# Performance work log

Hardware: AMD Instinct MI355X
Metric: run time of the kernel (lower is better)

## Reference

```python
import jax, jax.numpy as jnp
import numpy as np

B, I, C, H, QP, VP = 2, 1024, 16, 12, 4, 8
W_C = (2.0 / (9.0 * QP)) ** 0.5
W_L = (1.0 / 3.0) ** 0.5


def setup_inputs() -> dict:
    key = jax.random.key(0)
    ks = jax.random.split(key, 14)
    rn = lambda k, shape, s=1.0: (jax.random.normal(k, shape, dtype=jnp.float32) * s)
    return {
        "s": rn(ks[0], (B, I, C)),
        "z": rn(ks[1], (B, I, I, C)),
        "R": rn(ks[2], (B, I, 3, 3)),
        "t": rn(ks[3], (B, I, 3)),
        "Wq": rn(ks[4], (C, C * H), C ** -0.5),
        "Wk": rn(ks[5], (C, C * H), C ** -0.5),
        "Wv": rn(ks[6], (C, C * H), C ** -0.5),
        "Wb": rn(ks[7], (C, H), C ** -0.5),
        "Wqp": rn(ks[8], (C, 3 * QP * H), C ** -0.5),
        "Wkp": rn(ks[9], (C, 3 * QP * H), C ** -0.5),
        "Wvp": rn(ks[10], (C, 3 * VP * H), C ** -0.5),
        "gamma": rn(ks[11], (H,), 0.5),
        "Wout": rn(ks[12], (H * (2 * C + 4 * VP), C), (H * (2 * C + 4 * VP)) ** -0.5),
        "bout": rn(ks[13], (C,), 0.02),
    }


def _apply_rigid(R, t, p):
    # p: (B, i, n, 3); rigid transform per residue: R @ p + t
    return jnp.einsum("bixy,bipy->bipx", R, p) + t[:, :, None, :]


def reference(s, z, R, t, Wq, Wk, Wv, Wb, Wqp, Wkp, Wvp, gamma, Wout, bout):
    b_, i_, c = s.shape
    h, qp, vp = gamma.shape[0], Wqp.shape[1] // (3 * gamma.shape[0]), Wvp.shape[1] // (3 * gamma.shape[0])

    q = (s @ Wq).reshape(b_, i_, h, c)
    k = (s @ Wk).reshape(b_, i_, h, c)
    v = (s @ Wv).reshape(b_, i_, h, c)

    q_pts = _apply_rigid(R, t, (s @ Wqp).reshape(b_, i_, h * qp, 3)).reshape(b_, i_, h, qp, 3)
    k_pts = _apply_rigid(R, t, (s @ Wkp).reshape(b_, i_, h * qp, 3)).reshape(b_, i_, h, qp, 3)
    v_pts = _apply_rigid(R, t, (s @ Wvp).reshape(b_, i_, h * vp, 3)).reshape(b_, i_, h, vp, 3)

    bias = jnp.einsum("bijc,ch->bhij", z, Wb)
    a = jnp.einsum("bihc,bjhc->bhij", q, k) * (c ** -0.5) + bias

    # squared point distances summed over points, expanded to avoid (B,i,j,h,P,3) tensor
    q2 = jnp.sum(q_pts ** 2, axis=(-1, -2))          # (B,i,h)
    k2 = jnp.sum(k_pts ** 2, axis=(-1, -2))          # (B,j,h)
    qk = jnp.einsum("bihpx,bjhpx->bhij", q_pts, k_pts)
    d2 = q2.transpose(0, 2, 1)[..., None] + k2.transpose(0, 2, 1)[:, :, None, :] - 2.0 * qk  # (B,h,i,j)

    head_w = jax.nn.softplus(gamma)                  # (h,)
    a = a + d2 * (head_w[None, :, None, None] * W_C * -0.5)
    a = a * W_L
    a = jax.nn.softmax(a, axis=-2)  # NOTE: original code softmaxes over dim=-2 (the i axis)

    # NOTE: original einsum indexes v by i (not j); replicated faithfully
    o = jnp.einsum("bhij,bihc->bihc", a, v).reshape(b_, i_, h * c)

    o_pts = jnp.einsum("bhij,bjhpx->bihpx", a, v_pts)  # (B,i,h,vp,3)
    o_pts_norm = jnp.sqrt(jnp.maximum(jnp.sum(o_pts ** 2, axis=-1), 1e-12)).reshape(b_, i_, h * vp)
    o_pts_flat = o_pts.reshape(b_, i_, h * vp * 3)

    o_pair = jnp.einsum("bhij,bijc->bihc", a, z).reshape(b_, i_, h * c)

    cat = jnp.concatenate([o, o_pair, o_pts_flat, o_pts_norm], axis=-1)
    return cat @ Wout + bout
```

## Files before the change

### kernel.cpp

```cpp
#include <hip/hip_runtime.h>
#include <hip/hip_bf16.h>
#include <math.h>

#define B_ 2
#define I_ 1024
#define C_ 16
#define H_ 12
#define ICH 8

__device__ __constant__ float kW_C = 0.23570226039551584f;
#define W_Lc 0.5773502691896258f
#define LOG2E 1.4426950408889634f

typedef _Float16 hf;
typedef hf hf2 __attribute__((ext_vector_type(2)));
typedef unsigned int u32;

template <typename T, typename F>
__device__ inline T bc(F f) { return __builtin_bit_cast(T, f); }

__device__ inline float fdot2f(u32 a, u32 b, float c) {
#if __has_builtin(__builtin_amdgcn_fdot2)
  return __builtin_amdgcn_fdot2(bc<hf2>(a), bc<hf2>(b), c, false);
#else
  hf2 x = bc<hf2>(a), y = bc<hf2>(b);
  return c + (float)x[0] * (float)y[0] + (float)x[1] * (float)y[1];
#endif
}

__device__ inline u32 pkrtz(float lo, float hi) {
#if __has_builtin(__builtin_amdgcn_cvt_pkrtz)
  return bc<u32>(__builtin_amdgcn_cvt_pkrtz(lo, hi));
#else
  hf2 t; t[0] = (hf)lo; t[1] = (hf)hi; return bc<u32>(t);
#endif
}

__device__ inline u32 permlo(u32 hiw, u32 low) {
#if __has_builtin(__builtin_amdgcn_perm)
  return __builtin_amdgcn_perm(hiw, low, 0x05040100u);
#else
  return (low & 0xffffu) | (hiw << 16);
#endif
}
__device__ inline u32 permhi(u32 hiw, u32 low) {
#if __has_builtin(__builtin_amdgcn_perm)
  return __builtin_amdgcn_perm(hiw, low, 0x07060302u);
#else
  return (low >> 16) | (hiw & 0xffff0000u);
#endif
}

__device__ inline void ld16lds(const ushort* p, u32* d) {
  const uint4* q = (const uint4*)p;
  uint4 a = q[0], b = q[1], c = q[2], e = q[3];
  d[0]=a.x; d[1]=a.y; d[2]=a.z; d[3]=a.w;
  d[4]=b.x; d[5]=b.y; d[6]=b.z; d[7]=b.w;
  d[8]=c.x; d[9]=c.y; d[10]=c.z; d[11]=c.w;
  d[12]=e.x; d[13]=e.y; d[14]=e.z; d[15]=e.w;
}
__device__ inline void ld8lds(const ushort* p, u32* d) {
  const uint4* q = (const uint4*)p;
  uint4 a = q[0], b = q[1];
  d[0]=a.x; d[1]=a.y; d[2]=a.z; d[3]=a.w;
  d[4]=b.x; d[5]=b.y; d[6]=b.z; d[7]=b.w;
}

#define QF16_OFF 0
#define QF16_SZ (B_*I_*196)
#define KF16_OFF (QF16_OFF + QF16_SZ)
#define KF16_SZ QF16_SZ
#define VPF_OFF (KF16_OFF + KF16_SZ)
#define VPF_SZ (B_*I_*144)
#define VV_OFF (VPF_OFF + VPF_SZ)
#define VV_SZ (B_*I_*192)
#define SM_OFF (VV_OFF + VV_SZ)
#define SM_SZ (B_*12*1024*2)
#define PM_OFF (SM_OFF + SM_SZ)
#define PM_SZ (B_*64*ICH*192*2)
#define LT_OFF (PM_OFF + PM_SZ)
#define LT_SZ (B_*H_*512*1024)
#define ACC2_OFF (LT_OFF + LT_SZ)

__global__ __launch_bounds__(192) void kA(const float* __restrict__ s, const float* __restrict__ R,
                 const float* __restrict__ t, const float* __restrict__ Wq,
                 const float* __restrict__ Wk, const float* __restrict__ Wv,
                 const float* __restrict__ Wqp, const float* __restrict__ Wkp,
                 const float* __restrict__ Wvp, const float* __restrict__ gam,
                 float* __restrict__ ws) {
  int blk = blockIdx.x;
  int b = blk >> 10, i = blk & 1023;
  int tid = threadIdx.x;
  __shared__ float sl[16], rl[9], tl[3], part[96];
  if (tid < 16) sl[tid] = s[(b*I_ + i)*C_ + tid];
  else if (tid < 25) rl[tid-16] = R[(size_t)(b*I_+i)*9 + (tid-16)];
  else if (tid < 28) tl[tid-25] = t[(size_t)(b*I_+i)*3 + (tid-25)];
  __syncthreads();
  hf* QF  = (hf*)(ws + QF16_OFF) + (size_t)(b*I_+i)*392;
  hf* KF  = (hf*)(ws + KF16_OFF) + (size_t)(b*I_+i)*392;
  ushort* VPP = (ushort*)(ws + VPF_OFF);
  float* vv = ws + VV_OFF + (size_t)(b*I_+i)*192;
  {
    int hc = tid; int h = hc >> 4, c = hc & 15;
    float aq = 0.f, ak = 0.f, av = 0.f;
    #pragma unroll
    for (int ci = 0; ci < 16; ci++) {
      float sv = sl[ci];
      aq += sv * Wq[ci*192 + hc];
      ak += sv * Wk[ci*192 + hc];
      av += sv * Wv[ci*192 + hc];
    }
    const float s_qk = 0.25f * W_Lc * LOG2E;
    QF[h*32 + c] = (hf)(aq * s_qk);
    KF[h*32 + c] = (hf)ak;
    vv[hc] = av;
  }
  {
    float raw[3], px[3];
    if (tid < 96) {
      bool isq = tid < 48;
      int n = isq ? tid : tid - 48;
      const float* W = isq ? Wqp : Wkp;
      #pragma unroll
      for (int x = 0; x < 3; x++) {
        float a2 = 0.f;
        #pragma unroll
        for (int ci = 0; ci < 16; ci++) a2 += sl[ci] * W[ci*144 + n*3 + x];
        raw[x] = a2;
      }
      #pragma unroll
      for (int x = 0; x < 3; x++)
        px[x] = rl[x*3]*raw[0] + rl[x*3+1]*raw[1] + rl[x*3+2]*raw[2] + tl[x];
      int h = n >> 2, p = n & 3;
      part[tid] = px[0]*px[0] + px[1]*px[1] + px[2]*px[2];
      if (isq) {
        float g = gam[h];
        float sp = log1pf(expf(g));
        float coef2 = -0.5f * kW_C * sp * W_Lc * LOG2E;
        #pragma unroll
        for (int x = 0; x < 3; x++) QF[h*32 + 16 + p*3 + x] = (hf)(px[x] * (-2.0f * coef2));
      } else {
        #pragma unroll
        for (int x = 0; x < 3; x++) KF[h*32 + 16 + p*3 + x] = (hf)px[x];
      }
    } else {
      int n = tid - 96;
      #pragma unroll
      for (int x = 0; x < 3; x++) {
        float a2 = 0.f;
        #pragma unroll
        for (int ci = 0; ci < 16; ci++) a2 += sl[ci] * Wvp[ci*288 + n*3 + x];
        raw[x] = a2;
      }
      #pragma unroll
      for (int x = 0; x < 3; x++)
        px[x] = rl[x*3]*raw[0] + rl[x*3+1]*raw[1] + rl[x*3+2]*raw[2] + tl[x];
      int h = n >> 3, p = n & 7;
      size_t base = ((size_t)(b*512 + (i >> 1))*12 + h)*48 + (i & 1);
      #pragma unroll
      for (int x = 0; x < 3; x++) VPP[base + (p*3 + x)*2] = bc<ushort>((hf)px[x]);
    }
  }
  __syncthreads();
  if (tid < 24) {
    int h = tid % 12; bool isq = tid < 12;
    float g = gam[h];
    float sp = log1pf(expf(g));
    float coef2 = -0.5f * kW_C * sp * W_Lc * LOG2E;
    float s2 = 0.f;
    int base = isq ? h*4 : 48 + h*4;
    #pragma unroll
    for (int p = 0; p < 4; p++) s2 += part[base + p];
    if (isq) {
      QF[h*32 + 28] = (hf)(coef2 * s2);
      QF[h*32 + 29] = (hf)1.0f;
      QF[h*32 + 30] = (hf)0.0f;
      QF[h*32 + 31] = (hf)0.0f;
    } else {
      KF[h*32 + 28] = (hf)1.0f;
      KF[h*32 + 29] = (hf)(coef2 * s2);
      KF[h*32 + 30] = (hf)0.0f;
      KF[h*32 + 31] = (hf)0.0f;
    }
  }
}

__global__ __launch_bounds__(192,4) void kB(const float* __restrict__ z,
                 const float* __restrict__ Wb, float* __restrict__ ws) {
  int blk = blockIdx.x;
  int ic = blk & (ICH-1); int jt = (blk >> 3) & 63; int b = blk >> 9;
  int tid = threadIdx.x; int h = tid >> 4, jl = tid & 15;
  int j = jt*16 + jl;
  __shared__ ushort qlds[16*392];
  __shared__ ushort zlds[16*392];
  __shared__ u32 llog[96*18];
  u32 kf[16];
  {
    const ushort* KF = (const ushort*)(ws + KF16_OFF) + (size_t)(b*I_+j)*392 + h*32;
    ld16lds(KF, kf);
  }
  u32 wb2[8];
  #pragma unroll
  for (int p = 0; p < 8; p++)
    wb2[p] = pkrtz(Wb[(2*p)*12 + h] * (W_Lc*LOG2E), Wb[(2*p+1)*12 + h] * (W_Lc*LOG2E));
  u32* LTu_w = (u32*)(ws + LT_OFF);
  float m = -1e30f, S = 0.f;
  int ibase = ic*128;
  for (int t = 0; t < 8; ++t) {
    int i0 = ibase + t*16;
    __syncthreads();
    {
      const uint4* qsrc = (const uint4*)((const hf*)(ws + QF16_OFF) + (size_t)(b*I_+i0)*392);
      uint4* qdst = (uint4*)qlds;
      for (int idx = tid; idx < 784; idx += 192) qdst[idx] = qsrc[idx];
    }
    for (int idx = tid; idx < 1024; idx += 192) {
      int r = idx >> 6, jj = (idx >> 2) & 15, c4 = idx & 3;
      float4 v = *(const float4*)(z + ((size_t)(b*I_ + i0 + r)*I_ + jt*16 + jj)*16 + c4*4);
      uint2 pk = make_uint2(pkrtz(v.x, v.y), pkrtz(v.z, v.w));
      *(uint2*)&zlds[r*392 + jj*24 + c4*4] = pk;
    }
    __syncthreads();
    u32 lw[8];
    #pragma unroll 1
    for (int ip = 0; ip < 8; ++ip) {
      u32 q0[16], q1[16], z0[8], z1[8];
      ld16lds(&qlds[(2*ip)*392 + h*32], q0);
      ld16lds(&qlds[(2*ip+1)*392 + h*32], q1);
      ld8lds(&zlds[(2*ip)*392 + jl*24], z0);
      ld8lds(&zlds[(2*ip+1)*392 + jl*24], z1);
      float a0 = 0.f, a1 = 0.f, b0 = 0.f, b1 = 0.f;
      #pragma unroll
      for (int p = 0; p < 16; p += 2) {
        a0 = fdot2f(q0[p], kf[p], a0);
        b0 = fdot2f(q0[p+1], kf[p+1], b0);
        a1 = fdot2f(q1[p], kf[p], a1);
        b1 = fdot2f(q1[p+1], kf[p+1], b1);
      }
      #pragma unroll
      for (int p = 0; p < 8; p += 2) {
        a0 = fdot2f(z0[p], wb2[p], a0);
        b0 = fdot2f(z0[p+1], wb2[p+1], b0);
        a1 = fdot2f(z1[p], wb2[p], a1);
        b1 = fdot2f(z1[p+1], wb2[p+1], b1);
      }
      float l0 = (a0 + b0), l1 = (a1 + b1);
      u32 w = pkrtz(l0, l1);
      lw[ip] = w;
      u32 pw = (u32)__shfl_xor((int)w, 1);
      u32 ex = (jl & 1) ? permhi(w, pw) : permlo(pw, w);
      llog[(h*8 + (jl>>1))*18 + 2*ip + (jl&1)] = ex;
    }
    {
      float l[16];
      #pragma unroll
      for (int p = 0; p < 8; p++) { hf2 lh = bc<hf2>(lw[p]); l[2*p] = (float)lh[0]; l[2*p+1] = (float)lh[1]; }
      float m8[8];
      #pragma unroll
      for (int p = 0; p < 8; p++) m8[p] = fmaxf(l[2*p], l[2*p+1]);
      float mt = fmaxf(fmaxf(fmaxf(m8[0],m8[1]), fmaxf(m8[2],m8[3])),
                       fmaxf(fmaxf(m8[4],m8[5]), fmaxf(m8[6],m8[7])));
      float e[16];
      #pragma unroll
      for (int p = 0; p < 16; p++) e[p] = __builtin_amdgcn_exp2f(l[p] - mt);
      float st = ((e[0]+e[1])+(e[2]+e[3])) + ((e[4]+e[5])+(e[6]+e[7]))
               + ((e[8]+e[9])+(e[10]+e[11])) + ((e[12]+e[13])+(e[14]+e[15]));
      float mn = fmaxf(m, mt);
      S = S * __builtin_amdgcn_exp2f(m - mn) + st * __builtin_amdgcn_exp2f(mt - mn);
      m = mn;
    }
    __syncthreads();
    {
      int row = tid >> 1, iseg = (tid & 1) << 3;
      int hh = row >> 3, jpg2 = row & 7;
      const u32* lr = llog + row*18 + iseg;
      u32 o0=lr[0],o1=lr[1],o2=lr[2],o3=lr[3],o4=lr[4],o5=lr[5],o6=lr[6],o7=lr[7];
      u32* dst = LTu_w + ((size_t)(b*12+hh)*512 + jt*8 + jpg2)*1024 + i0 + iseg;
      *(uint4*)dst = make_uint4(o0,o1,o2,o3);
      *(uint4*)(dst+4) = make_uint4(o4,o5,o6,o7);
    }
  }
  float2* pm = (float2*)(ws + PM_OFF);
  pm[((size_t)(b*64+jt)*ICH + ic)*192 + tid] = make_float2(m, S);
}

__global__ __launch_bounds__(192) void kB2(float* __restrict__ ws) {
  int blk = blockIdx.x; int jt = blk & 63, b = blk >> 6;
  int tid = threadIdx.x; int h = tid >> 4, jl = tid & 15;
  const float2* pm = (const float2*)(ws + PM_OFF) + (size_t)(b*64+jt)*ICH*192 + tid;
  float m = -1e30f, S = 0.f;
  #pragma unroll
  for (int ic = 0; ic < ICH; ic++) {
    float2 p = pm[ic*192];
    float mn = fmaxf(m, p.x);
    S = S * __builtin_amdgcn_exp2f(m - mn) + p.y * __builtin_amdgcn_exp2f(p.x - mn);
    m = mn;
  }
  int j = jt*16 + jl;
  float* sm = ws + SM_OFF + ((size_t)((b*12+h)*1024) + j)*2;
  sm[0] = m;
  sm[1] = 1.0f / S;
}

__global__ __launch_bounds__(192,6) void kC(const float* __restrict__ z,
                 float* __restrict__ ws, int jsh) {
  int blk = blockIdx.x;
  int jch = 1 << jsh;
  int jc = blk & (jch-1); int it = (blk >> jsh) & 63; int b = blk >> (jsh+6);
  int tid = threadIdx.x; int h = tid >> 4, il = tid & 15;
  int i = it*16 + il;
  __shared__ u32 llds[96*18];
  __shared__ u32 zplds[16*132];
  float opts[24], opair[16], rsum = 0.f;
  #pragma unroll
  for (int n = 0; n < 24; n++) opts[n] = 0.f;
  #pragma unroll
  for (int c = 0; c < 16; c++) opair[c] = 0.f;
  const u32* LTu = (const u32*)(ws + LT_OFF);
  const float* SM = ws + SM_OFF + (size_t)((b*12+h)*1024)*2;
  const ushort* VPP = (const ushort*)(ws + VPF_OFF);
  int chunk = I_ >> jsh;
  int nt = chunk >> 4;
  int hh = tid >> 4, rr = tid & 15, sjp = rr >> 1, sq = rr & 1;
  for (int t = 0; t < nt; ++t) {
    int j0 = jc*chunk + t*16;
    int jpg0 = j0 >> 1;
    __syncthreads();
    {
      const u32* src = LTu + ((size_t)(b*12+hh)*512 + jpg0 + sjp)*1024 + it*16 + sq*8;
      uint4 a = *(const uint4*)src;
      uint4 c4 = *(const uint4*)(src + 4);
      u32* drow = llds + (hh*8 + sjp)*18 + sq*8;
      *(uint2*)(drow + 0) = make_uint2(a.x, a.y);
      *(uint2*)(drow + 2) = make_uint2(a.z, a.w);
      *(uint2*)(drow + 4) = make_uint2(c4.x, c4.y);
      *(uint2*)(drow + 6) = make_uint2(c4.z, c4.w);
    }
    for (int idx = tid; idx < 512; idx += 192) {
      int r = idx >> 5, jp = (idx >> 2) & 7, c4 = idx & 3;
      const float* zb = z + ((size_t)(b*I_ + it*16 + r)*I_ + j0 + 2*jp)*16 + c4*4;
      float4 a = *(const float4*)zb;
      float4 d = *(const float4*)(zb + 16);
      uint4 o = make_uint4(pkrtz(a.x, d.x), pkrtz(a.y, d.y), pkrtz(a.z, d.z), pkrtz(a.w, d.w));
      *(uint4*)&zplds[r*132 + jp*16 + c4*4] = o;
    }
    __syncthreads();
    #pragma unroll 1
    for (int jp = 0; jp < 8; ++jp) {
      u32 lp = llds[(h*8 + jp)*18 + il];
      float4 st = *(const float4*)(SM + (size_t)(j0 + 2*jp)*2);
      const uint4* vp4 = (const uint4*)(VPP + ((size_t)(b*512 + jpg0 + jp)*12 + h)*48);
      uint4 va = vp4[0], vb = vp4[1], vc = vp4[2];
      uint4 vd = vp4[3], ve = vp4[4], vf = vp4[5];
      hf2 lh = bc<hf2>(lp);
      float w0 = __builtin_amdgcn_exp2f((float)lh[0] - st.x) * st.y;
      float w1 = __builtin_amdgcn_exp2f((float)lh[1] - st.z) * st.w;
      rsum += w0 + w1;
      u32 w2 = pkrtz(w0, w1);
      const u32* zr = &zplds[il*132 + jp*16];
      uint4 p0 = *(const uint4*)(zr + 0), p1 = *(const uint4*)(zr + 4);
      uint4 p2 = *(const uint4*)(zr + 8), p3 = *(const uint4*)(zr + 12);
      opair[0]  = fdot2f(w2, p0.x, opair[0]);
      opair[1]  = fdot2f(w2, p0.y, opair[1]);
      opair[2]  = fdot2f(w2, p0.z, opair[2]);
      opair[3]  = fdot2f(w2, p0.w, opair[3]);
      opair[4]  = fdot2f(w2, p1.x, opair[4]);
      opair[5]  = fdot2f(w2, p1.y, opair[5]);
      opair[6]  = fdot2f(w2, p1.z, opair[6]);
      opair[7]  = fdot2f(w2, p1.w, opair[7]);
      opair[8]  = fdot2f(w2, p2.x, opair[8]);
      opair[9]  = fdot2f(w2, p2.y, opair[9]);
      opair[10] = fdot2f(w2, p2.z, opair[10]);
      opair[11] = fdot2f(w2, p2.w, opair[11]);
      opair[12] = fdot2f(w2, p3.x, opair[12]);
      opair[13] = fdot2f(w2, p3.y, opair[13]);
      opair[14] = fdot2f(w2, p3.z, opair[14]);
      opair[15] = fdot2f(w2, p3.w, opair[15]);
      opts[0]  = fdot2f(w2, va.x, opts[0]);
      opts[1]  = fdot2f(w2, va.y, opts[1]);
      opts[2]  = fdot2f(w2, va.z, opts[2]);
      opts[3]  = fdot2f(w2, va.w, opts[3]);
      opts[4]  = fdot2f(w2, vb.x, opts[4]);
      opts[5]  = fdot2f(w2, vb.y, opts[5]);
      opts[6]  = fdot2f(w2, vb.z, opts[6]);
      opts[7]  = fdot2f(w2, vb.w, opts[7]);
      opts[8]  = fdot2f(w2, vc.x, opts[8]);
      opts[9]  = fdot2f(w2, vc.y, opts[9]);
      opts[10] = fdot2f(w2, vc.z, opts[10]);
      opts[11] = fdot2f(w2, vc.w, opts[11]);
      opts[12] = fdot2f(w2, vd.x, opts[12]);
      opts[13] = fdot2f(w2, vd.y, opts[13]);
      opts[14] = fdot2f(w2, vd.z, opts[14]);
      opts[15] = fdot2f(w2, vd.w, opts[15]);
      opts[16] = fdot2f(w2, ve.x, opts[16]);
      opts[17] = fdot2f(w2, ve.y, opts[17]);
      opts[18] = fdot2f(w2, ve.z, opts[18]);
      opts[19] = fdot2f(w2, ve.w, opts[19]);
      opts[20] = fdot2f(w2, vf.x, opts[20]);
      opts[21] = fdot2f(w2, vf.y, opts[21]);
      opts[22] = fdot2f(w2, vf.z, opts[22]);
      opts[23] = fdot2f(w2, vf.w, opts[23]);
    }
  }
  ushort* ab = (ushort*)(ws + ACC2_OFF) + ((size_t)(b*I_+i)*jch + jc)*512;
  #pragma unroll
  for (int n = 0; n < 24; n++) ab[h*24 + n] = bc<ushort>((hf)opts[n]);
  #pragma unroll
  for (int c = 0; c < 16; c++) ab[288 + h*16 + c] = bc<ushort>((hf)opair[c]);
  ab[480 + h] = bc<ushort>((hf)rsum);
}

__global__ __launch_bounds__(256) void kD(const float* __restrict__ Wout, const float* __restrict__ bout,
                 const float* __restrict__ ws, float* __restrict__ out, int jsh) {
  int jch = 1 << jsh;
  int blk = blockIdx.x;
  int b = blk >> 8; int i0 = (blk & 255) << 2;
  int tid = threadIdx.x;
  __shared__ float accs[4*512];
  __shared__ float cat[4*776];
  __shared__ float red[256];
  const ushort* ACC2us = (const ushort*)(ws + ACC2_OFF);
  for (int idx = tid; idx < 4*512; idx += 256) {
    int r = idx >> 9, f = idx & 511;
    const ushort* src = ACC2us + (size_t)(b*I_+i0+r)*jch*512 + f;
    float ssum = 0.f;
    for (int jc = 0; jc < jch; jc++) ssum += (float)bc<hf>(src[jc*512]);
    accs[idx] = ssum;
  }
  __syncthreads();
  const float* vv = ws + VV_OFF;
  for (int idx = tid; idx < 4*768; idx += 256) {
    int r = idx / 768, f = idx - r*768;
    int i = i0 + r;
    const float* ab = accs + r*512;
    float val;
    if (f < 192) {
      int h = f >> 4, c = f & 15;
      val = vv[(size_t)(b*I_+i)*192 + h*16 + c] * ab[480 + h];
    } else if (f < 384) {
      val = ab[288 + (f - 192)];
    } else if (f < 672) {
      val = ab[f - 384];
    } else {
      int g = f - 672; int base = (g >> 3)*24 + (g & 7)*3;
      float x0 = ab[base], x1 = ab[base+1], x2 = ab[base+2];
      val = sqrtf(fmaxf(x0*x0 + x1*x1 + x2*x2, 1e-12f));
    }
    cat[r*776 + f] = val;
  }
  __syncthreads();
  {
    int r = tid >> 6, c = (tid >> 2) & 15, sseg = tid & 3;
    const float* cr = cat + r*776;
    float a = 0.f;
    for (int f = sseg*192; f < sseg*192 + 192; f++) a += cr[f] * Wout[f*16 + c];
    red[tid] = a;
  }
  __syncthreads();
  if ((tid & 3) == 0) {
    int r = tid >> 6, c = (tid >> 2) & 15;
    float sum = bout[c] + red[tid] + red[tid+1] + red[tid+2] + red[tid+3];
    out[((size_t)(b*I_) + i0 + r)*16 + c] = sum;
  }
}

extern "C" void kernel_launch(void* const* d_in, const int* in_sizes, int n_in,
                              void* d_out, int out_size, void* d_ws, size_t ws_size,
                              hipStream_t stream) {
  const float* s    = (const float*)d_in[0];
  const float* z    = (const float*)d_in[1];
  const float* R    = (const float*)d_in[2];
  const float* t    = (const float*)d_in[3];
  const float* Wq   = (const float*)d_in[4];
  const float* Wk   = (const float*)d_in[5];
  const float* Wv   = (const float*)d_in[6];
  const float* Wb   = (const float*)d_in[7];
  const float* Wqp  = (const float*)d_in[8];
  const float* Wkp  = (const float*)d_in[9];
  const float* Wvp  = (const float*)d_in[10];
  const float* gam  = (const float*)d_in[11];
  const float* Wout = (const float*)d_in[12];
  const float* bout = (const float*)d_in[13];
  float* out = (float*)d_out;
  float* ws = (float*)d_ws;

  int jsh = 4;
  while (jsh > 0) {
    size_t need = ((size_t)ACC2_OFF + (size_t)B_*I_*(1u<<jsh)*256) * 4u;
    if (need <= ws_size) break;
    jsh--;
  }

  hipLaunchKernelGGL(kA, dim3(B_*I_), dim3(192), 0, stream,
                     s, R, t, Wq, Wk, Wv, Wqp, Wkp, Wvp, gam, ws);
  hipLaunchKernelGGL(kB, dim3(B_*64*ICH), dim3(192), 0, stream, z, Wb, ws);
  hipLaunchKernelGGL(kB2, dim3(B_*64), dim3(192), 0, stream, ws);
  hipLaunchKernelGGL(kC, dim3(B_*64*(1<<jsh)), dim3(192), 0, stream, z, ws, jsh);
  hipLaunchKernelGGL(kD, dim3(B_*256), dim3(256), 0, stream, Wout, bout, ws, out, jsh);
}
```

Measured before the change: 193.4 us.

## Compute attention logits and pair bias in kB with MFMA instructions

Replaces the per-thread fdot2 loops in kB with MFMA matrix instructions: a 16x16x32 f16 MFMA for the q·k feature dot products and a 16x16x16 MFMA for the z·Wb pair bias. The block grows to 256 threads (four waves) and results are staged through new LDS buffers before the softmax statistics and transposed logit writes. It is meant to cut the scalar dot-product ALU cost of the logit pass, in exchange for an extra barrier, more LDS traffic and idle threads in the softmax phase. Logits are now summed in fp32 before rounding to f16, so rounding differs slightly from before.

```diff
diff --git a/kernel.cpp b/kernel.cpp
--- a/kernel.cpp
+++ b/kernel.cpp
@@ -14,6 +14,9 @@
 
 typedef _Float16 hf;
 typedef hf hf2 __attribute__((ext_vector_type(2)));
+typedef hf hf4v __attribute__((ext_vector_type(4)));
+typedef hf hf8v __attribute__((ext_vector_type(8)));
+typedef float f32x4 __attribute__((ext_vector_type(4)));
 typedef unsigned int u32;
 
 template <typename T, typename F>
@@ -49,21 +52,6 @@
 #else
   return (low >> 16) | (hiw & 0xffff0000u);
 #endif
-}
-
-__device__ inline void ld16lds(const ushort* p, u32* d) {
-  const uint4* q = (const uint4*)p;
-  uint4 a = q[0], b = q[1], c = q[2], e = q[3];
-  d[0]=a.x; d[1]=a.y; d[2]=a.z; d[3]=a.w;
-  d[4]=b.x; d[5]=b.y; d[6]=b.z; d[7]=b.w;
-  d[8]=c.x; d[9]=c.y; d[10]=c.z; d[11]=c.w;
-  d[12]=e.x; d[13]=e.y; d[14]=e.z; d[15]=e.w;
-}
-__device__ inline void ld8lds(const ushort* p, u32* d) {
-  const uint4* q = (const uint4*)p;
-  uint4 a = q[0], b = q[1];
-  d[0]=a.x; d[1]=a.y; d[2]=a.z; d[3]=a.w;
-  d[4]=b.x; d[5]=b.y; d[6]=b.z; d[7]=b.w;
 }
 
 #define QF16_OFF 0
@@ -185,103 +173,119 @@
   }
 }
 
-__global__ __launch_bounds__(192,4) void kB(const float* __restrict__ z,
+__global__ __launch_bounds__(256,4) void kB(const float* __restrict__ z,
                  const float* __restrict__ Wb, float* __restrict__ ws) {
   int blk = blockIdx.x;
   int ic = blk & (ICH-1); int jt = (blk >> 3) & 63; int b = blk >> 9;
-  int tid = threadIdx.x; int h = tid >> 4, jl = tid & 15;
-  int j = jt*16 + jl;
+  int tid = threadIdx.x;
+  int w = tid >> 6, lane = tid & 63;
+  int ln15 = lane & 15, l16 = lane >> 4;
+  int j0 = jt*16;
   __shared__ ushort qlds[16*392];
-  __shared__ ushort zlds[16*392];
-  __shared__ u32 llog[96*18];
-  u32 kf[16];
-  {
-    const ushort* KF = (const ushort*)(ws + KF16_OFF) + (size_t)(b*I_+j)*392 + h*32;
-    ld16lds(KF, kf);
-  }
-  u32 wb2[8];
-  #pragma unroll
-  for (int p = 0; p < 8; p++)
-    wb2[p] = pkrtz(Wb[(2*p)*12 + h] * (W_Lc*LOG2E), Wb[(2*p+1)*12 + h] * (W_Lc*LOG2E));
+  __shared__ u32 lqk[12*16*18];
+  __shared__ ushort lbias[16*208];
+  __shared__ u32 llog[96*17];
+  hf8v kf[3];
+  #pragma unroll
+  for (int q = 0; q < 3; q++) {
+    int h = w*3 + q;
+    const ushort* src = (const ushort*)(ws + KF16_OFF) + ((size_t)(b*I_ + j0 + ln15)*392 + h*32 + l16*8);
+    kf[q] = *(const hf8v*)src;
+  }
+  hf4v wbf;
+  #pragma unroll
+  for (int e = 0; e < 4; e++) {
+    int c = l16*4 + e;
+    float v = (ln15 < 12) ? Wb[c*12 + ln15] * (W_Lc*LOG2E) : 0.f;
+    wbf[e] = (hf)v;
+  }
   u32* LTu_w = (u32*)(ws + LT_OFF);
   float m = -1e30f, S = 0.f;
-  int ibase = ic*128;
   for (int t = 0; t < 8; ++t) {
-    int i0 = ibase + t*16;
+    int i0 = ic*128 + t*16;
     __syncthreads();
     {
       const uint4* qsrc = (const uint4*)((const hf*)(ws + QF16_OFF) + (size_t)(b*I_+i0)*392);
       uint4* qdst = (uint4*)qlds;
-      for (int idx = tid; idx < 784; idx += 192) qdst[idx] = qsrc[idx];
-    }
-    for (int idx = tid; idx < 1024; idx += 192) {
-      int r = idx >> 6, jj = (idx >> 2) & 15, c4 = idx & 3;
-      float4 v = *(const float4*)(z + ((size_t)(b*I_ + i0 + r)*I_ + jt*16 + jj)*16 + c4*4);
-      uint2 pk = make_uint2(pkrtz(v.x, v.y), pkrtz(v.z, v.w));
-      *(uint2*)&zlds[r*392 + jj*24 + c4*4] = pk;
+      for (int idx = tid; idx < 784; idx += 256) qdst[idx] = qsrc[idx];
     }
     __syncthreads();
-    u32 lw[8];
-    #pragma unroll 1
-    for (int ip = 0; ip < 8; ++ip) {
-      u32 q0[16], q1[16], z0[8], z1[8];
-      ld16lds(&qlds[(2*ip)*392 + h*32], q0);
-      ld16lds(&qlds[(2*ip+1)*392 + h*32], q1);
-      ld8lds(&zlds[(2*ip)*392 + jl*24], z0);
-      ld8lds(&zlds[(2*ip+1)*392 + jl*24], z1);
-      float a0 = 0.f, a1 = 0.f, b0 = 0.f, b1 = 0.f;
-      #pragma unroll
-      for (int p = 0; p < 16; p += 2) {
-        a0 = fdot2f(q0[p], kf[p], a0);
-        b0 = fdot2f(q0[p+1], kf[p+1], b0);
-        a1 = fdot2f(q1[p], kf[p], a1);
-        b1 = fdot2f(q1[p+1], kf[p+1], b1);
+    #pragma unroll
+    for (int q = 0; q < 3; q++) {
+      int h = w*3 + q;
+      hf8v a = *(const hf8v*)&qlds[ln15*392 + h*32 + l16*8];
+      f32x4 c = {0.f, 0.f, 0.f, 0.f};
+      c = __builtin_amdgcn_mfma_f32_16x16x32_f16(a, kf[q], c, 0, 0, 0);
+      u32* dst = &lqk[(h*16 + ln15)*18 + l16*4];
+      *(uint2*)dst     = make_uint2(bc<u32>(c[0]), bc<u32>(c[1]));
+      *(uint2*)(dst+2) = make_uint2(bc<u32>(c[2]), bc<u32>(c[3]));
+    }
+    #pragma unroll
+    for (int r = 0; r < 4; r++) {
+      int ii = w*4 + r;
+      float4 zv = *(const float4*)(z + ((size_t)(b*I_ + i0 + ii)*I_ + j0 + ln15)*16 + l16*4);
+      uint2 ap = make_uint2(pkrtz(zv.x, zv.y), pkrtz(zv.z, zv.w));
+      hf4v a = bc<hf4v>(ap);
+      f32x4 cb = {0.f, 0.f, 0.f, 0.f};
+      cb = __builtin_amdgcn_mfma_f32_16x16x16f16(a, wbf, cb, 0, 0, 0);
+      if (ln15 < 12) {
+        #pragma unroll
+        for (int reg = 0; reg < 4; reg++) {
+          int jj = l16*4 + reg;
+          lbias[ii*208 + jj*13 + ln15] = bc<ushort>((hf)cb[reg]);
+        }
       }
-      #pragma unroll
-      for (int p = 0; p < 8; p += 2) {
-        a0 = fdot2f(z0[p], wb2[p], a0);
-        b0 = fdot2f(z0[p+1], wb2[p+1], b0);
-        a1 = fdot2f(z1[p], wb2[p], a1);
-        b1 = fdot2f(z1[p+1], wb2[p+1], b1);
-      }
-      float l0 = (a0 + b0), l1 = (a1 + b1);
-      u32 w = pkrtz(l0, l1);
-      lw[ip] = w;
-      u32 pw = (u32)__shfl_xor((int)w, 1);
-      u32 ex = (jl & 1) ? permhi(w, pw) : permlo(pw, w);
-      llog[(h*8 + (jl>>1))*18 + 2*ip + (jl&1)] = ex;
-    }
-    {
+    }
+    __syncthreads();
+    if (tid < 192) {
+      int h = tid >> 4, jl = tid & 15;
+      const u32* qk = &lqk[(h*16 + jl)*18];
       float l[16];
       #pragma unroll
-      for (int p = 0; p < 8; p++) { hf2 lh = bc<hf2>(lw[p]); l[2*p] = (float)lh[0]; l[2*p+1] = (float)lh[1]; }
+      for (int i = 0; i < 16; i++) l[i] = bc<float>(qk[i]);
+      #pragma unroll
+      for (int i = 0; i < 16; i++) l[i] += (float)bc<hf>(lbias[i*208 + jl*13 + h]);
+      u32 lw[8];
+      #pragma unroll
+      for (int p = 0; p < 8; p++) lw[p] = pkrtz(l[2*p], l[2*p+1]);
+      float lr[16];
+      #pragma unroll
+      for (int p = 0; p < 8; p++) { hf2 lh = bc<hf2>(lw[p]); lr[2*p] = (float)lh[0]; lr[2*p+1] = (float)lh[1]; }
       float m8[8];
       #pragma unroll
-      for (int p = 0; p < 8; p++) m8[p] = fmaxf(l[2*p], l[2*p+1]);
+      for (int p = 0; p < 8; p++) m8[p] = fmaxf(lr[2*p], lr[2*p+1]);
       float mt = fmaxf(fmaxf(fmaxf(m8[0],m8[1]), fmaxf(m8[2],m8[3])),
                        fmaxf(fmaxf(m8[4],m8[5]), fmaxf(m8[6],m8[7])));
       float e[16];
       #pragma unroll
-      for (int p = 0; p < 16; p++) e[p] = __builtin_amdgcn_exp2f(l[p] - mt);
+      for (int p = 0; p < 16; p++) e[p] = __builtin_amdgcn_exp2f(lr[p] - mt);
       float st = ((e[0]+e[1])+(e[2]+e[3])) + ((e[4]+e[5])+(e[6]+e[7]))
                + ((e[8]+e[9])+(e[10]+e[11])) + ((e[12]+e[13])+(e[14]+e[15]));
       float mn = fmaxf(m, mt);
       S = S * __builtin_amdgcn_exp2f(m - mn) + st * __builtin_amdgcn_exp2f(mt - mn);
       m = mn;
+      #pragma unroll
+      for (int p = 0; p < 8; p++) {
+        u32 pw = (u32)__shfl_xor((int)lw[p], 1);
+        u32 ex = (jl & 1) ? permhi(lw[p], pw) : permlo(pw, lw[p]);
+        llog[(h*8 + (jl>>1))*17 + 2*p + (jl&1)] = ex;
+      }
     }
     __syncthreads();
-    {
+    if (tid < 192) {
       int row = tid >> 1, iseg = (tid & 1) << 3;
+      const u32* lr2 = &llog[row*17 + iseg];
+      u32 o0=lr2[0],o1=lr2[1],o2=lr2[2],o3=lr2[3],o4=lr2[4],o5=lr2[5],o6=lr2[6],o7=lr2[7];
       int hh = row >> 3, jpg2 = row & 7;
-      const u32* lr = llog + row*18 + iseg;
-      u32 o0=lr[0],o1=lr[1],o2=lr[2],o3=lr[3],o4=lr[4],o5=lr[5],o6=lr[6],o7=lr[7];
       u32* dst = LTu_w + ((size_t)(b*12+hh)*512 + jt*8 + jpg2)*1024 + i0 + iseg;
       *(uint4*)dst = make_uint4(o0,o1,o2,o3);
       *(uint4*)(dst+4) = make_uint4(o4,o5,o6,o7);
     }
   }
-  float2* pm = (float2*)(ws + PM_OFF);
-  pm[((size_t)(b*64+jt)*ICH + ic)*192 + tid] = make_float2(m, S);
+  if (tid < 192) {
+    float2* pm = (float2*)(ws + PM_OFF);
+    pm[((size_t)(b*64+jt)*ICH + ic)*192 + tid] = make_float2(m, S);
+  }
 }
 
 __global__ __launch_bounds__(192) void kB2(float* __restrict__ ws) {
@@ -493,7 +497,7 @@
 
   hipLaunchKernelGGL(kA, dim3(B_*I_), dim3(192), 0, stream,
                      s, R, t, Wq, Wk, Wv, Wqp, Wkp, Wvp, gam, ws);
-  hipLaunchKernelGGL(kB, dim3(B_*64*ICH), dim3(192), 0, stream, z, Wb, ws);
+  hipLaunchKernelGGL(kB, dim3(B_*64*ICH), dim3(256), 0, stream, z, Wb, ws);
   hipLaunchKernelGGL(kB2, dim3(B_*64), dim3(192), 0, stream, ws);
   hipLaunchKernelGGL(kC, dim3(B_*64*(1<<jsh)), dim3(192), 0, stream, z, ws, jsh);
   hipLaunchKernelGGL(kD, dim3(B_*256), dim3(256), 0, stream, Wout, bout, ws, out, jsh);
```

After: 172.9 us. -10.6%, faster.
